# Optimization experiments

Measured on AMD Instinct MI355X. Metric: run time of the kernel, lower is better.

## Reference

```python
import jax, jax.numpy as jnp
import numpy as np

T, B, H, K = 512, 64, 512, 16  # seq_len, batch, hidden_size, num_tags


def setup_inputs() -> dict:
    key = jax.random.key(0)
    ks = jax.random.split(key, 8)
    hidden = jax.random.normal(ks[0], (T, B, H), dtype=jnp.float32)
    W1 = jax.random.normal(ks[1], (H, H), dtype=jnp.float32) / np.float32(np.sqrt(H))
    b1 = jnp.zeros((H,), jnp.float32)
    W2 = jax.random.normal(ks[2], (H, K), dtype=jnp.float32) / np.float32(np.sqrt(H))
    b2 = jnp.zeros((K,), jnp.float32)
    transition = jax.random.normal(ks[3], (K, K), dtype=jnp.float32)
    lens = jax.random.randint(ks[4], (B,), T // 2, T + 1)  # valid lengths in [T/2, T]
    tags = jax.random.randint(ks[5], (T, B), 0, K)
    return dict(hidden=hidden, W1=W1, b1=b1, W2=W2, b2=b2,
                transition=transition, lens=lens, tags=tags)


def reference(hidden, W1, b1, W2, b2, transition, lens, tags):
    # Emission MLP (dropout is identity in eval): Linear -> ReLU -> Linear
    h = jax.nn.relu(hidden @ W1 + b1)          # [T, B, H]
    em = h @ W2 + b2                           # [T, B, K]

    # ---- forward (partition) score: linear-chain logsumexp DP ----
    def step(alpha, e_t):
        # alpha: [B, K] over prev tags; transition[curr, prev]
        a = jax.nn.logsumexp(alpha[:, None, :] + transition[None, :, :], axis=-1) + e_t
        return a, a

    alpha0 = em[0]
    _, alphas = jax.lax.scan(step, alpha0, em[1:])
    alphas = jnp.concatenate([alpha0[None], alphas], axis=0)            # [T, B, K]
    last = jnp.take_along_axis(alphas, (lens - 1)[None, :, None], axis=0)[0]  # [B, K]
    fwd_score = jax.nn.logsumexp(last, axis=-1)                          # [B]

    # ---- gold path score ----
    em_path = jnp.take_along_axis(em, tags[:, :, None], axis=-1)[..., 0]  # [T, B]
    trans_path = transition[tags[1:], tags[:-1]]                          # [T-1, B]
    steps = em_path.at[1:].add(trans_path)
    cum = jnp.cumsum(steps, axis=0)                                       # [T, B]
    gold = jnp.take_along_axis(cum, (lens - 1)[None, :], axis=0)[0]       # [B]

    return (fwd_score - gold).sum()
```

## Files before the change

### kernel.cpp

```cpp
#include <hip/hip_runtime.h>
#include <hip/hip_bf16.h>

#define TT 512
#define BB 64
#define HH 512
#define KK 16

typedef __attribute__((ext_vector_type(8))) short bf16x8;
typedef __attribute__((ext_vector_type(4))) short bf16x4;
typedef __attribute__((ext_vector_type(4))) float f32x4;

#define MFMA_K16(A, B, C) __builtin_amdgcn_mfma_f32_16x16x16bf16_1k(A, B, C, 0, 0, 0)

__device__ __forceinline__ unsigned short f2bf(float f) {
    union { __hip_bfloat16 h; unsigned short u; } cvt;
    cvt.h = __float2bfloat16(f);
    return cvt.u;
}

__device__ __forceinline__ short rne_bf(float x) {
    unsigned u = __float_as_uint(x);
    u += 0x7fffu + ((u >> 16) & 1u);
    return (short)(u >> 16);
}

__device__ __forceinline__ float bf2f(short s) {
    return __uint_as_float(((unsigned)(unsigned short)s) << 16);
}

__global__ void prep_kernel(const float* __restrict__ W1, const float* __restrict__ W2,
                            unsigned short* __restrict__ W1t, unsigned short* __restrict__ W2t,
                            float* __restrict__ out) {
    const int bi = blockIdx.x, tx = threadIdx.x;
    if (bi < 64) {
        __shared__ float Ls[64][65];
        const int ti = bi & 7, tj = bi >> 3;
        const int r0 = ti * 64, c0 = tj * 64;
        const int r = tx >> 4, c4 = (tx & 15) * 4;
#pragma unroll
        for (int i = 0; i < 4; ++i) {
            float4 v = *(const float4*)(W1 + (size_t)(r0 + r + 16 * i) * HH + c0 + c4);
            Ls[c4 + 0][r + 16 * i] = v.x;
            Ls[c4 + 1][r + 16 * i] = v.y;
            Ls[c4 + 2][r + 16 * i] = v.z;
            Ls[c4 + 3][r + 16 * i] = v.w;
        }
        __syncthreads();
        const int rn = tx >> 4, k4 = (tx & 15) * 4;
#pragma unroll
        for (int i = 0; i < 4; ++i) {
            const int n = rn + 16 * i;
            ushort4 o;
            o.x = f2bf(Ls[n][k4 + 0]);
            o.y = f2bf(Ls[n][k4 + 1]);
            o.z = f2bf(Ls[n][k4 + 2]);
            o.w = f2bf(Ls[n][k4 + 3]);
            *(ushort4*)(W1t + (size_t)(c0 + n) * HH + r0 + k4) = o;
        }
    } else {
        if (tx == 0) out[0] = 0.0f;
        for (int idx = tx; idx < 16 * HH; idx += 256) {
            const int n = idx >> 9, k = idx & 511;
            W2t[idx] = f2bf(W2[k * KK + n]);
        }
    }
}

__global__ __launch_bounds__(256, 2)
void em_kernel(const float* __restrict__ hidden, const unsigned short* __restrict__ W1t,
               const float* __restrict__ b1, const unsigned short* __restrict__ W2t,
               const float* __restrict__ b2, float* __restrict__ em) {
    __shared__ unsigned short W2ts[16 * 520];
    __shared__ __align__(16) unsigned char stage[37888];
    unsigned short* As = (unsigned short*)stage;
    unsigned short* Bs = (unsigned short*)(stage + 5120);
    unsigned short* Hb = (unsigned short*)stage;

    const int tx = threadIdx.x;
    const int w = tx >> 6, lane = tx & 63;
    const int q = lane >> 4, nl = lane & 15;
    const int wm = w >> 1, wn = w & 1;
    const int row0 = blockIdx.x * 64;

    for (int i = tx; i < 16 * 64; i += 256) {
        const int n = i >> 6, kc = i & 63;
        *(bf16x8*)(W2ts + n * 520 + kc * 8) = *(const bf16x8*)(W2t + n * HH + kc * 8);
    }

    f32x4 acc[2][16];
#pragma unroll
    for (int mt = 0; mt < 2; ++mt)
#pragma unroll
        for (int nt = 0; nt < 16; ++nt) acc[mt][nt] = (f32x4){0.f, 0.f, 0.f, 0.f};

    for (int kt = 0; kt < 16; ++kt) {
        const int k0 = kt * 32;
        __syncthreads();
        {
            const int r = tx >> 2, c8 = (tx & 3) * 8;
            const float* src = hidden + (size_t)(row0 + r) * HH + k0 + c8;
            float4 v0 = *(const float4*)(src);
            float4 v1 = *(const float4*)(src + 4);
            bf16x8 o;
            o[0] = (short)f2bf(v0.x); o[1] = (short)f2bf(v0.y);
            o[2] = (short)f2bf(v0.z); o[3] = (short)f2bf(v0.w);
            o[4] = (short)f2bf(v1.x); o[5] = (short)f2bf(v1.y);
            o[6] = (short)f2bf(v1.z); o[7] = (short)f2bf(v1.w);
            *(bf16x8*)(As + r * 40 + c8) = o;
        }
#pragma unroll
        for (int it = 0; it < 8; ++it) {
            const int c = it * 256 + tx;
            const int n = c >> 2, slot = c & 3;
            const int kc = slot ^ ((n >> 1) & 3);
            __builtin_amdgcn_global_load_lds(
                (const __attribute__((address_space(1))) void*)(W1t + (size_t)n * HH + k0 + kc * 8),
                (__attribute__((address_space(3))) void*)(Bs + c * 8),
                16, 0, 0);
        }
        __syncthreads();
        bf16x8 af[2];
#pragma unroll
        for (int mt = 0; mt < 2; ++mt)
            af[mt] = *(const bf16x8*)(As + (32 * wm + 16 * mt + nl) * 40 + q * 8);
#pragma unroll
        for (int nt = 0; nt < 16; ++nt) {
            const int n = 256 * wn + 16 * nt + nl;
            const int slot = q ^ ((n >> 1) & 3);
            bf16x8 bf = *(const bf16x8*)(Bs + n * 32 + slot * 8);
            acc[0][nt] = __builtin_amdgcn_mfma_f32_16x16x32_bf16(af[0], bf, acc[0][nt], 0, 0, 0);
            acc[1][nt] = __builtin_amdgcn_mfma_f32_16x16x32_bf16(af[1], bf, acc[1][nt], 0, 0, 0);
        }
    }

    f32x4 acc2 = (f32x4){0.f, 0.f, 0.f, 0.f};
    for (int c = 0; c < 2; ++c) {
        __syncthreads();
        if (wn == c) {
#pragma unroll
            for (int nt = 0; nt < 16; ++nt) {
                const float bv = b1[c * 256 + 16 * nt + nl];
#pragma unroll
                for (int mt = 0; mt < 2; ++mt) {
#pragma unroll
                    for (int r = 0; r < 4; ++r) {
                        float v = acc[mt][nt][r] + bv;
                        v = v > 0.f ? v : 0.f;
                        const int row = 32 * wm + 16 * mt + q * 4 + r;
                        Hb[row * 264 + nt * 16 + nl] = f2bf(v);
                    }
                }
            }
        }
        __syncthreads();
#pragma unroll
        for (int ks = 0; ks < 8; ++ks) {
            bf16x8 a2 = *(const bf16x8*)(Hb + (16 * w + nl) * 264 + ks * 32 + q * 8);
            bf16x8 b2f = *(const bf16x8*)(W2ts + nl * 520 + c * 256 + ks * 32 + q * 8);
            acc2 = __builtin_amdgcn_mfma_f32_16x16x32_bf16(a2, b2f, acc2, 0, 0, 0);
        }
    }
#pragma unroll
    for (int r = 0; r < 4; ++r) {
        const int row = row0 + 16 * w + q * 4 + r;
        em[(size_t)row * KK + nl] = acc2[r] + b2[nl];
    }
}

__global__ void gold_kernel(const float* __restrict__ em, const float* __restrict__ trans,
                            const int* __restrict__ lens, const int* __restrict__ tags,
                            float* __restrict__ out) {
    __shared__ float trs[256];
    __shared__ float red[4];
    const int tid = threadIdx.x;
    trs[tid] = __logf(bf2f(rne_bf(__expf(trans[tid]))));
    __syncthreads();
    const int idx = blockIdx.x * 256 + tid;
    const int t = idx >> 6, b = idx & 63;
    const int L = lens[b];
    float v = 0.0f;
    if (t < L) {
        const int tg = tags[t * BB + b];
        v = em[((size_t)t * BB + b) * KK + tg];
        if (t > 0) v += trs[tg * 16 + tags[(t - 1) * BB + b]];
    }
#pragma unroll
    for (int dd = 1; dd < 64; dd <<= 1) v += __shfl_xor(v, dd, 64);
    if ((tid & 63) == 0) red[tid >> 6] = v;
    __syncthreads();
    if (tid == 0) atomicAdd(out, -(red[0] + red[1] + red[2] + red[3]));
}

__global__ void chunk_kernel(const float* __restrict__ em, const float* __restrict__ trans,
                             const int* __restrict__ lens,
                             float* __restrict__ Pfull, float* __restrict__ Cfull,
                             float* __restrict__ Ppart, float* __restrict__ Cpart) {
    const int tx = threadIdx.x;
    const int id = blockIdx.x * 4 + (tx >> 6);
    const int lane = tx & 63, q = lane >> 4, col = lane & 15;
    const int b = id >> 3, c = id & 7;

    float mf[4];
    {
        float4 tv = *(const float4*)(trans + col * 16 + 4 * q);
        mf[0] = bf2f(rne_bf(__expf(tv.x)));
        mf[1] = bf2f(rne_bf(__expf(tv.y)));
        mf[2] = bf2f(rne_bf(__expf(tv.z)));
        mf[3] = bf2f(rne_bf(__expf(tv.w)));
    }
    const int Lm1 = lens[b] - 1;
    const int tb0 = 64 * c;

    float ebuf[8];
#pragma unroll
    for (int i = 0; i < 8; ++i)
        ebuf[i] = em[(size_t)((tb0 + i) * BB + b) * KK + col];

    bf16x4 gb;
#pragma unroll
    for (int i = 0; i < 4; ++i)
        gb[i] = (4 * q + i == col) ? rne_bf(1.0f) : (short)0;

    const f32x4 zc = (f32x4){0.f, 0.f, 0.f, 0.f};
    f32x4 d = (f32x4){0.f, 0.f, 0.f, 0.f};
    float K = 1.0f, rk = 1.0f, lk = 0.0f, Cacc = 0.0f;

    for (int sb = 0; sb < 64; sb += 8) {
        const bool refill = (sb < 56);
#pragma unroll
        for (int s8 = 0; s8 < 8; ++s8) {
            const int t = tb0 + sb + s8;
            const float eraw = ebuf[s8];
            if (refill)
                ebuf[s8] = em[(size_t)((t + 8) * BB + b) * KK + col];
            float ev = __expf(eraw);
            if ((s8 & 3) == 0 && (sb + s8) >= 4) {
                ev *= rk;
                Cacc += lk;
            }
            bf16x4 af;
            af[0] = rne_bf(ev * mf[0]); af[1] = rne_bf(ev * mf[1]);
            af[2] = rne_bf(ev * mf[2]); af[3] = rne_bf(ev * mf[3]);
            if (s8 == 0) {
                if (sb == 0 && c == 0) {
#pragma unroll
                    for (int i = 0; i < 4; ++i)
                        af[i] = (4 * q + i == col) ? rne_bf(ev) : (short)0;
                }
            }
            d = MFMA_K16(af, gb, zc);
            if ((s8 & 3) == 1) {
                K = __shfl(d[0], 0, 64);
                const float Km = fmaxf(K, 1e-30f);
                rk = 1.0f / Km;
                lk = __logf(Km);
            }
            if (t == Lm1) {
#pragma unroll
                for (int r = 0; r < 4; ++r)
                    Ppart[b * 256 + (4 * q + r) * 16 + col] = d[r];
                if (lane == 0) Cpart[b] = Cacc;
            }
            gb[0] = rne_bf(d[0]); gb[1] = rne_bf(d[1]);
            gb[2] = rne_bf(d[2]); gb[3] = rne_bf(d[3]);
        }
    }
#pragma unroll
    for (int r = 0; r < 4; ++r)
        Pfull[(size_t)(b * 8 + c) * 256 + (4 * q + r) * 16 + col] = d[r];
    if (lane == 0) Cfull[b * 8 + c] = Cacc;
}

__global__ void combine_kernel(const int* __restrict__ lens,
                               const float* __restrict__ Pfull, const float* __restrict__ Cfull,
                               const float* __restrict__ Ppart, const float* __restrict__ Cpart,
                               float* __restrict__ out) {
    const int lane = threadIdx.x;
    const int grp = lane >> 4, j = lane & 15;
    const int b = blockIdx.x * 4 + grp;
    const int base = grp << 4;
    const int cstar = (lens[b] - 1) >> 6;

    float g = 1.0f, acc = 0.0f;
    for (int c = 0; c < 8; ++c) {
        const bool act = (c <= cstar);
        const float* P = (c < cstar) ? (Pfull + (size_t)(b * 8 + c) * 256)
                                     : (Ppart + b * 256);
        float gn = 0.0f;
#pragma unroll
        for (int k = 0; k < 16; ++k) {
            const float gk = __shfl(g, base + k, 64);
            gn += P[j * 16 + k] * gk;
        }
        if (act) {
            float m = gn;
#pragma unroll
            for (int dd = 1; dd < 16; dd <<= 1) m = fmaxf(m, __shfl_xor(m, dd, 64));
            g = gn / m;
            acc += __logf(m) + ((c < cstar) ? Cfull[b * 8 + c] : Cpart[b]);
        }
    }
    float ssum = g;
#pragma unroll
    for (int dd = 1; dd < 16; dd <<= 1) ssum += __shfl_xor(ssum, dd, 64);
    const float fwd = acc + __logf(ssum);
    if (j == 0) atomicAdd(out, fwd);
}

extern "C" void kernel_launch(void* const* d_in, const int* in_sizes, int n_in,
                              void* d_out, int out_size, void* d_ws, size_t ws_size,
                              hipStream_t stream) {
    const float* hidden = (const float*)d_in[0];
    const float* W1     = (const float*)d_in[1];
    const float* b1     = (const float*)d_in[2];
    const float* W2     = (const float*)d_in[3];
    const float* b2     = (const float*)d_in[4];
    const float* trans  = (const float*)d_in[5];
    const int*   lens   = (const int*)d_in[6];
    const int*   tags   = (const int*)d_in[7];
    float* out = (float*)d_out;

    char* ws = (char*)d_ws;
    float* em = (float*)ws;
    unsigned short* W1t = (unsigned short*)(ws + 2097152);
    unsigned short* W2t = (unsigned short*)(ws + 2621440);
    float* Pfull = (float*)(ws + 2637824);
    float* Cfull = (float*)(ws + 3162112);
    float* Ppart = (float*)(ws + 3164160);
    float* Cpart = (float*)(ws + 3229696);

    prep_kernel<<<65, 256, 0, stream>>>(W1, W2, W1t, W2t, out);
    em_kernel<<<512, 256, 0, stream>>>(hidden, W1t, b1, W2t, b2, em);
    gold_kernel<<<128, 256, 0, stream>>>(em, trans, lens, tags, out);
    chunk_kernel<<<128, 256, 0, stream>>>(em, trans, lens, Pfull, Cfull, Ppart, Cpart);
    combine_kernel<<<16, 64, 0, stream>>>(lens, Pfull, Cfull, Ppart, Cpart, out);
}
```

Before: 165.1 us.

## Fuse pipeline into cooperative persistent kernel and shorten forward-DP chunks

Merges prep, emission GEMM, chunked forward DP and combine into one cooperative kernel separated by grid syncs, with a multi-kernel fallback. The gold-score kernel is folded into the per-batch combine. Chunk length in the DP drops from 64 to 16 steps, giving 2048 independent chunk tasks instead of 512, and full-chunk transfer matrices are stored as bf16. The aim is to cut launch overhead and expose more parallelism in the serial DP. The cost is grid-sync latency, a combine loop four times longer (32 chunks per batch), and extra rounding error from the bf16 matrices.

Result: slower. 359.5 us (+117.7%).

```diff
diff --git a/kernel.cpp b/kernel.cpp
--- a/kernel.cpp
+++ b/kernel.cpp
@@ -1,5 +1,8 @@
 #include <hip/hip_runtime.h>
+#include <hip/hip_cooperative_groups.h>
 #include <hip/hip_bf16.h>
+
+namespace cg = cooperative_groups;
 
 #define TT 512
 #define BB 64
@@ -11,6 +14,7 @@
 typedef __attribute__((ext_vector_type(4))) float f32x4;
 
 #define MFMA_K16(A, B, C) __builtin_amdgcn_mfma_f32_16x16x16bf16_1k(A, B, C, 0, 0, 0)
+#define MFMA_K32(A, B, C) __builtin_amdgcn_mfma_f32_16x16x32_bf16(A, B, C, 0, 0, 0)
 
 __device__ __forceinline__ unsigned short f2bf(float f) {
     union { __hip_bfloat16 h; unsigned short u; } cvt;
@@ -28,12 +32,12 @@
     return __uint_as_float(((unsigned)(unsigned short)s) << 16);
 }
 
-__global__ void prep_kernel(const float* __restrict__ W1, const float* __restrict__ W2,
-                            unsigned short* __restrict__ W1t, unsigned short* __restrict__ W2t,
-                            float* __restrict__ out) {
-    const int bi = blockIdx.x, tx = threadIdx.x;
+
+__device__ __forceinline__ void do_prep(int bi, int tx,
+        const float* W1, const float* W2,
+        unsigned short* W1t, unsigned short* W2t, float* out,
+        float (*Ls)[65]) {
     if (bi < 64) {
-        __shared__ float Ls[64][65];
         const int ti = bi & 7, tj = bi >> 3;
         const int r0 = ti * 64, c0 = tj * 64;
         const int r = tx >> 4, c4 = (tx & 15) * 4;
@@ -57,7 +61,7 @@
             o.w = f2bf(Ls[n][k4 + 3]);
             *(ushort4*)(W1t + (size_t)(c0 + n) * HH + r0 + k4) = o;
         }
-    } else {
+    } else if (bi == 64) {
         if (tx == 0) out[0] = 0.0f;
         for (int idx = tx; idx < 16 * HH; idx += 256) {
             const int n = idx >> 9, k = idx & 511;
@@ -66,26 +70,25 @@
     }
 }
 
-__global__ __launch_bounds__(256, 2)
-void em_kernel(const float* __restrict__ hidden, const unsigned short* __restrict__ W1t,
-               const float* __restrict__ b1, const unsigned short* __restrict__ W2t,
-               const float* __restrict__ b2, float* __restrict__ em) {
-    __shared__ unsigned short W2ts[16 * 520];
-    __shared__ __align__(16) unsigned char stage[37888];
+__device__ __forceinline__ void do_stage_w2(int tx, const unsigned short* W2t,
+                                            unsigned short* W2ts) {
+    for (int i = tx; i < 16 * 64; i += 256) {
+        const int n = i >> 6, kc = i & 63;
+        *(bf16x8*)(W2ts + n * 520 + kc * 8) = *(const bf16x8*)(W2t + n * HH + kc * 8);
+    }
+}
+
+__device__ __forceinline__ void do_em_tile(int row0, int tx,
+        const float* hidden, const unsigned short* W1t,
+        const float* b1, const float* b2, float* em,
+        const unsigned short* W2ts, unsigned char* stage) {
     unsigned short* As = (unsigned short*)stage;
     unsigned short* Bs = (unsigned short*)(stage + 5120);
     unsigned short* Hb = (unsigned short*)stage;
 
-    const int tx = threadIdx.x;
     const int w = tx >> 6, lane = tx & 63;
     const int q = lane >> 4, nl = lane & 15;
     const int wm = w >> 1, wn = w & 1;
-    const int row0 = blockIdx.x * 64;
-
-    for (int i = tx; i < 16 * 64; i += 256) {
-        const int n = i >> 6, kc = i & 63;
-        *(bf16x8*)(W2ts + n * 520 + kc * 8) = *(const bf16x8*)(W2t + n * HH + kc * 8);
-    }
 
     f32x4 acc[2][16];
 #pragma unroll
@@ -128,8 +131,8 @@
             const int n = 256 * wn + 16 * nt + nl;
             const int slot = q ^ ((n >> 1) & 3);
             bf16x8 bf = *(const bf16x8*)(Bs + n * 32 + slot * 8);
-            acc[0][nt] = __builtin_amdgcn_mfma_f32_16x16x32_bf16(af[0], bf, acc[0][nt], 0, 0, 0);
-            acc[1][nt] = __builtin_amdgcn_mfma_f32_16x16x32_bf16(af[1], bf, acc[1][nt], 0, 0, 0);
+            acc[0][nt] = MFMA_K32(af[0], bf, acc[0][nt]);
+            acc[1][nt] = MFMA_K32(af[1], bf, acc[1][nt]);
         }
     }
 
@@ -157,7 +160,7 @@
         for (int ks = 0; ks < 8; ++ks) {
             bf16x8 a2 = *(const bf16x8*)(Hb + (16 * w + nl) * 264 + ks * 32 + q * 8);
             bf16x8 b2f = *(const bf16x8*)(W2ts + nl * 520 + c * 256 + ks * 32 + q * 8);
-            acc2 = __builtin_amdgcn_mfma_f32_16x16x32_bf16(a2, b2f, acc2, 0, 0, 0);
+            acc2 = MFMA_K32(a2, b2f, acc2);
         }
     }
 #pragma unroll
@@ -167,38 +170,11 @@
     }
 }
 
-__global__ void gold_kernel(const float* __restrict__ em, const float* __restrict__ trans,
-                            const int* __restrict__ lens, const int* __restrict__ tags,
-                            float* __restrict__ out) {
-    __shared__ float trs[256];
-    __shared__ float red[4];
-    const int tid = threadIdx.x;
-    trs[tid] = __logf(bf2f(rne_bf(__expf(trans[tid]))));
-    __syncthreads();
-    const int idx = blockIdx.x * 256 + tid;
-    const int t = idx >> 6, b = idx & 63;
-    const int L = lens[b];
-    float v = 0.0f;
-    if (t < L) {
-        const int tg = tags[t * BB + b];
-        v = em[((size_t)t * BB + b) * KK + tg];
-        if (t > 0) v += trs[tg * 16 + tags[(t - 1) * BB + b]];
-    }
-#pragma unroll
-    for (int dd = 1; dd < 64; dd <<= 1) v += __shfl_xor(v, dd, 64);
-    if ((tid & 63) == 0) red[tid >> 6] = v;
-    __syncthreads();
-    if (tid == 0) atomicAdd(out, -(red[0] + red[1] + red[2] + red[3]));
-}
-
-__global__ void chunk_kernel(const float* __restrict__ em, const float* __restrict__ trans,
-                             const int* __restrict__ lens,
-                             float* __restrict__ Pfull, float* __restrict__ Cfull,
-                             float* __restrict__ Ppart, float* __restrict__ Cpart) {
-    const int tx = threadIdx.x;
-    const int id = blockIdx.x * 4 + (tx >> 6);
-    const int lane = tx & 63, q = lane >> 4, col = lane & 15;
-    const int b = id >> 3, c = id & 7;
+__device__ __forceinline__ void do_chunk(int id, int lane,
+        const float* em, const float* trans, const int* lens,
+        unsigned short* Pfull, float* Cfull, float* Ppart, float* Cpart) {
+    const int q = lane >> 4, col = lane & 15;
+    const int c = id >> 6, b = id & 63;
 
     float mf[4];
     {
@@ -209,7 +185,7 @@
         mf[3] = bf2f(rne_bf(__expf(tv.w)));
     }
     const int Lm1 = lens[b] - 1;
-    const int tb0 = 64 * c;
+    const int tb0 = 16 * c;
 
     float ebuf[8];
 #pragma unroll
@@ -225,8 +201,8 @@
     f32x4 d = (f32x4){0.f, 0.f, 0.f, 0.f};
     float K = 1.0f, rk = 1.0f, lk = 0.0f, Cacc = 0.0f;
 
-    for (int sb = 0; sb < 64; sb += 8) {
-        const bool refill = (sb < 56);
+    for (int sb = 0; sb < 16; sb += 8) {
+        const bool refill = (sb == 0);
 #pragma unroll
         for (int s8 = 0; s8 < 8; ++s8) {
             const int t = tb0 + sb + s8;
@@ -241,12 +217,10 @@
             bf16x4 af;
             af[0] = rne_bf(ev * mf[0]); af[1] = rne_bf(ev * mf[1]);
             af[2] = rne_bf(ev * mf[2]); af[3] = rne_bf(ev * mf[3]);
-            if (s8 == 0) {
-                if (sb == 0 && c == 0) {
-#pragma unroll
-                    for (int i = 0; i < 4; ++i)
-                        af[i] = (4 * q + i == col) ? rne_bf(ev) : (short)0;
-                }
+            if (sb == 0 && s8 == 0 && c == 0) {
+#pragma unroll
+                for (int i = 0; i < 4; ++i)
+                    af[i] = (4 * q + i == col) ? rne_bf(ev) : (short)0;
             }
             d = MFMA_K16(af, gb, zc);
             if ((s8 & 3) == 1) {
@@ -267,44 +241,142 @@
     }
 #pragma unroll
     for (int r = 0; r < 4; ++r)
-        Pfull[(size_t)(b * 8 + c) * 256 + (4 * q + r) * 16 + col] = d[r];
-    if (lane == 0) Cfull[b * 8 + c] = Cacc;
-}
-
-__global__ void combine_kernel(const int* __restrict__ lens,
-                               const float* __restrict__ Pfull, const float* __restrict__ Cfull,
-                               const float* __restrict__ Ppart, const float* __restrict__ Cpart,
-                               float* __restrict__ out) {
-    const int lane = threadIdx.x;
-    const int grp = lane >> 4, j = lane & 15;
-    const int b = blockIdx.x * 4 + grp;
-    const int base = grp << 4;
-    const int cstar = (lens[b] - 1) >> 6;
-
-    float g = 1.0f, acc = 0.0f;
-    for (int c = 0; c < 8; ++c) {
-        const bool act = (c <= cstar);
-        const float* P = (c < cstar) ? (Pfull + (size_t)(b * 8 + c) * 256)
-                                     : (Ppart + b * 256);
-        float gn = 0.0f;
-#pragma unroll
-        for (int k = 0; k < 16; ++k) {
-            const float gk = __shfl(g, base + k, 64);
-            gn += P[j * 16 + k] * gk;
-        }
-        if (act) {
-            float m = gn;
-#pragma unroll
-            for (int dd = 1; dd < 16; dd <<= 1) m = fmaxf(m, __shfl_xor(m, dd, 64));
-            g = gn / m;
-            acc += __logf(m) + ((c < cstar) ? Cfull[b * 8 + c] : Cpart[b]);
-        }
-    }
-    float ssum = g;
-#pragma unroll
-    for (int dd = 1; dd < 16; dd <<= 1) ssum += __shfl_xor(ssum, dd, 64);
-    const float fwd = acc + __logf(ssum);
-    if (j == 0) atomicAdd(out, fwd);
+        Pfull[(size_t)(b * 32 + c) * 256 + (4 * q + r) * 16 + col] = (unsigned short)rne_bf(d[r]);
+    if (lane == 0) Cfull[b * 32 + c] = Cacc;
+}
+
+__device__ __forceinline__ void do_combine(int b, int tx,
+        const float* em, const float* trans, const int* lens, const int* tags,
+        const unsigned short* Pfull, const float* Cfull,
+        const float* Ppart, const float* Cpart,
+        float* out, float* lds260) {
+    float* trs = lds260;
+    float* red = lds260 + 256;
+    trs[tx] = __logf(bf2f(rne_bf(__expf(trans[tx]))));
+    __syncthreads();
+    const int L = lens[b];
+    float v = 0.0f;
+#pragma unroll
+    for (int p = 0; p < 2; ++p) {
+        const int t = p * 256 + tx;
+        if (t < L) {
+            const int tg = tags[t * BB + b];
+            float u = em[((size_t)t * BB + b) * KK + tg];
+            if (t > 0) u += trs[tg * 16 + tags[(t - 1) * BB + b]];
+            v += u;
+        }
+    }
+#pragma unroll
+    for (int dd = 1; dd < 64; dd <<= 1) v += __shfl_xor(v, dd, 64);
+    if ((tx & 63) == 0) red[tx >> 6] = v;
+    __syncthreads();
+
+    if (tx < 64) {
+        const int j = tx & 15;
+        const int base = (tx >> 4) << 4;
+        const int cstar = (L - 1) >> 4;
+        float g = 1.0f, acc = 0.0f;
+        for (int c = 0; c < 32; ++c) {
+            if (c <= cstar) {
+                float gn = 0.0f;
+                if (c < cstar) {
+                    const unsigned short* P = Pfull + (size_t)(b * 32 + c) * 256;
+#pragma unroll
+                    for (int k = 0; k < 16; ++k) {
+                        const float gk = __shfl(g, base + k, 64);
+                        gn += bf2f((short)P[j * 16 + k]) * gk;
+                    }
+                } else {
+                    const float* P = Ppart + b * 256;
+#pragma unroll
+                    for (int k = 0; k < 16; ++k) {
+                        const float gk = __shfl(g, base + k, 64);
+                        gn += P[j * 16 + k] * gk;
+                    }
+                }
+                float m = gn;
+#pragma unroll
+                for (int dd = 1; dd < 16; dd <<= 1) m = fmaxf(m, __shfl_xor(m, dd, 64));
+                g = gn / m;
+                acc += __logf(m) + ((c < cstar) ? Cfull[b * 32 + c] : Cpart[b]);
+            }
+        }
+        float ssum = g;
+#pragma unroll
+        for (int dd = 1; dd < 16; dd <<= 1) ssum += __shfl_xor(ssum, dd, 64);
+        const float fwd = acc + __logf(ssum);
+        if (tx == 0)
+            atomicAdd(out, fwd - (red[0] + red[1] + red[2] + red[3]));
+    }
+}
+
+__global__ __launch_bounds__(256, 2)
+void mega_kernel(const float* hidden, const float* W1, const float* b1,
+                 const float* W2, const float* b2, const float* trans,
+                 const int* lens, const int* tags, float* out,
+                 float* em, unsigned short* W1t, unsigned short* W2t,
+                 unsigned short* Pfull, float* Cfull, float* Ppart, float* Cpart) {
+    cg::grid_group grid = cg::this_grid();
+    __shared__ __align__(16) unsigned char smem[54528];
+    unsigned short* W2ts = (unsigned short*)smem;
+    unsigned char* stage = smem + 16640;
+
+    const int tx = threadIdx.x, bi = blockIdx.x, G = gridDim.x;
+
+    do_prep(bi, tx, W1, W2, W1t, W2t, out, (float (*)[65])stage);
+    __threadfence();
+    grid.sync();
+
+    do_stage_w2(tx, W2t, W2ts);
+    for (int rt = bi; rt < 512; rt += G)
+        do_em_tile(rt * 64, tx, hidden, W1t, b1, b2, em, W2ts, stage);
+    __threadfence();
+    grid.sync();
+
+    {
+        const int w4 = tx >> 6;
+        for (int id = bi * 4 + w4; id < 2048; id += G * 4)
+            do_chunk(id, tx & 63, em, trans, lens, Pfull, Cfull, Ppart, Cpart);
+    }
+    __threadfence();
+    grid.sync();
+
+    if (bi < 64)
+        do_combine(bi, tx, em, trans, lens, tags, Pfull, Cfull, Ppart, Cpart,
+                   out, (float*)smem);
+}
+
+__global__ __launch_bounds__(256)
+void prep_kernel(const float* W1, const float* W2,
+                 unsigned short* W1t, unsigned short* W2t, float* out) {
+    __shared__ float Ls[64][65];
+    do_prep(blockIdx.x, threadIdx.x, W1, W2, W1t, W2t, out, Ls);
+}
+
+__global__ __launch_bounds__(256, 2)
+void em_kernel(const float* hidden, const unsigned short* W1t, const float* b1,
+               const unsigned short* W2t, const float* b2, float* em) {
+    __shared__ __align__(16) unsigned char smem[54528];
+    unsigned short* W2ts = (unsigned short*)smem;
+    unsigned char* stage = smem + 16640;
+    do_stage_w2(threadIdx.x, W2t, W2ts);
+    do_em_tile(blockIdx.x * 64, threadIdx.x, hidden, W1t, b1, b2, em, W2ts, stage);
+}
+
+__global__ __launch_bounds__(256)
+void chunk_kernel(const float* em, const float* trans, const int* lens,
+                  unsigned short* Pfull, float* Cfull, float* Ppart, float* Cpart) {
+    do_chunk(blockIdx.x * 4 + (threadIdx.x >> 6), threadIdx.x & 63,
+             em, trans, lens, Pfull, Cfull, Ppart, Cpart);
+}
+
+__global__ __launch_bounds__(256)
+void combine_kernel(const float* em, const float* trans, const int* lens,
+                    const int* tags, const unsigned short* Pfull, const float* Cfull,
+                    const float* Ppart, const float* Cpart, float* out) {
+    __shared__ float lds260[320];
+    do_combine(blockIdx.x, threadIdx.x, em, trans, lens, tags,
+               Pfull, Cfull, Ppart, Cpart, out, lds260);
 }
 
 extern "C" void kernel_launch(void* const* d_in, const int* in_sizes, int n_in,
@@ -324,14 +396,35 @@
     float* em = (float*)ws;
     unsigned short* W1t = (unsigned short*)(ws + 2097152);
     unsigned short* W2t = (unsigned short*)(ws + 2621440);
-    float* Pfull = (float*)(ws + 2637824);
-    float* Cfull = (float*)(ws + 3162112);
-    float* Ppart = (float*)(ws + 3164160);
-    float* Cpart = (float*)(ws + 3229696);
-
-    prep_kernel<<<65, 256, 0, stream>>>(W1, W2, W1t, W2t, out);
-    em_kernel<<<512, 256, 0, stream>>>(hidden, W1t, b1, W2t, b2, em);
-    gold_kernel<<<128, 256, 0, stream>>>(em, trans, lens, tags, out);
-    chunk_kernel<<<128, 256, 0, stream>>>(em, trans, lens, Pfull, Cfull, Ppart, Cpart);
-    combine_kernel<<<16, 64, 0, stream>>>(lens, Pfull, Cfull, Ppart, Cpart, out);
-}
+    unsigned short* Pfull = (unsigned short*)(ws + 2097152);
+    float* Cfull = (float*)(ws + 3145728);
+    float* Ppart = (float*)(ws + 3153920);
+    float* Cpart = (float*)(ws + 3219456);
+
+    int dev = 0;
+    (void)hipGetDevice(&dev);
+    int coop = 0, ncu = 0, occ = 0;
+    (void)hipDeviceGetAttribute(&coop, hipDeviceAttributeCooperativeLaunch, dev);
+    (void)hipDeviceGetAttribute(&ncu, hipDeviceAttributeMultiprocessorCount, dev);
+    (void)hipOccupancyMaxActiveBlocksPerMultiprocessor(&occ, (const void*)mega_kernel, 256, 0);
+
+    long Gl = (long)occ * (long)ncu;
+    if (Gl > 512) Gl = 512;
+
+    hipError_t e = hipErrorUnknown;
+    if (coop && Gl >= 65) {
+        void* args[] = {(void*)&hidden, (void*)&W1, (void*)&b1, (void*)&W2, (void*)&b2,
+                        (void*)&trans, (void*)&lens, (void*)&tags, (void*)&out,
+                        (void*)&em, (void*)&W1t, (void*)&W2t,
+                        (void*)&Pfull, (void*)&Cfull, (void*)&Ppart, (void*)&Cpart};
+        e = hipLaunchCooperativeKernel((const void*)mega_kernel, dim3((unsigned)Gl),
+                                       dim3(256), args, 0, stream);
+    }
+    if (e != hipSuccess) {
+        prep_kernel<<<65, 256, 0, stream>>>(W1, W2, W1t, W2t, out);
+        em_kernel<<<512, 256, 0, stream>>>(hidden, W1t, b1, W2t, b2, em);
+        chunk_kernel<<<512, 256, 0, stream>>>(em, trans, lens, Pfull, Cfull, Ppart, Cpart);
+        combine_kernel<<<64, 256, 0, stream>>>(em, trans, lens, tags,
+                                               Pfull, Cfull, Ppart, Cpart, out);
+    }
+}
```
